# Kernel optimization log

Hardware: AMD Instinct MI355X
Metric: run time of the kernel (lower is better)

Reference implementation:

```python
import jax, jax.numpy as jnp
import numpy as np

B = 1048576
EPS = 1e-5

def _lin_params(key, din, dout):
    k1, k2 = jax.random.split(key)
    bound = 1.0 / np.sqrt(din)
    w = jax.random.uniform(k1, (din, dout), minval=-bound, maxval=bound, dtype=jnp.float32)
    b = jax.random.uniform(k2, (dout,), minval=-bound, maxval=bound, dtype=jnp.float32)
    return w, b

def setup_inputs() -> dict:
    key = jax.random.key(0)
    ks = jax.random.split(key, 10)
    x = jax.random.normal(ks[0], (B, 8), dtype=jnp.float32)
    dims = [(8, 16), (16, 16), (16, 12), (12, 8), (8, 4), (4, 4), (4, 4), (4, 1)]
    names = ['fm', 'c1', 'p1', 'c2', 'p2', 'c3', 'r', 'h']
    inp = {'x': x,
           'bn_g': jnp.ones((8,), jnp.float32),
           'bn_b': jnp.zeros((8,), jnp.float32)}
    for i, (nm, (di, do)) in enumerate(zip(names, dims)):
        w, b = _lin_params(ks[i + 1], di, do)
        inp['w_' + nm] = w
        inp['b_' + nm] = b
    return inp

def reference(x, bn_g, bn_b, w_fm, b_fm, w_c1, b_c1, w_p1, b_p1, w_c2, b_c2,
              w_p2, b_p2, w_c3, b_c3, w_r, b_r, w_h, b_h):
    # BatchNorm1d (training mode): batch statistics, biased variance
    mu = jnp.mean(x, axis=0)
    var = jnp.mean((x - mu) ** 2, axis=0)
    h = (x - mu) * jax.lax.rsqrt(var + EPS) * bn_g + bn_b
    h = jnp.tanh(h @ w_fm + b_fm)   # [B,16] feature_map
    h = jnp.tanh(h @ w_c1 + b_c1)   # [B,16] conv1
    h = jnp.tanh(h @ w_p1 + b_p1)   # [B,12] pool1
    h = jnp.tanh(h @ w_c2 + b_c2)   # [B,8]  conv2
    h = jnp.tanh(h @ w_p2 + b_p2)   # [B,4]  pool2
    h = jnp.tanh(h @ w_c3 + b_c3)   # [B,4]  conv3
    res = jax.nn.relu(h @ w_r + b_r)  # [B,4] residual branch
    h = h + res
    return jax.nn.sigmoid(h @ w_h + b_h)  # [B,1]
```

## Files before the change

### kernel.cpp

```cpp
#include <hip/hip_runtime.h>
#include <stdint.h>

#define B_ROWS 1048576
#define ROWS_PER_THREAD 2
#define MAIN_BLOCKS (B_ROWS / (256 * ROWS_PER_THREAD))
#define STAT_BLOCKS 1024

typedef __fp16 h2 __attribute__((ext_vector_type(2)));

#define PART_OFF 16
#define WPK_OFF 16400
#define BIA_OFF 16770
#define W_FM 0
#define W_C1 64
#define W_P1 192
#define W_C2 288
#define W_P2 336
#define W_C3 352
#define W_R  360
#define W_H  368
#define B_FM 0
#define B_C1 16
#define B_P1 32
#define B_C2 44
#define B_P2 52
#define B_C3 56
#define B_R  60
#define B_H  64

__device__ __forceinline__ float exp_tanh(float x) {
    float e = __builtin_amdgcn_exp2f(x * 2.8853900817779268f);
    return 1.0f - 2.0f * __builtin_amdgcn_rcpf(e + 1.0f);
}

__device__ __forceinline__ float fast_sigmoid(float x) {
    float e = __builtin_amdgcn_exp2f(x * -1.4426950408889634f);
    return __builtin_amdgcn_rcpf(1.0f + e);
}

__global__ __launch_bounds__(256) void bn_stats(const float* __restrict__ x,
                                                float* __restrict__ ws) {
    const int tid = blockIdx.x * 256 + threadIdx.x;
    float s[8], q[8];
#pragma unroll
    for (int c = 0; c < 8; ++c) { s[c] = 0.f; q[c] = 0.f; }
    const float4* x4 = (const float4*)x;
#pragma unroll
    for (int k = 0; k < 4; ++k) {
        int r = tid + k * 262144;
        float4 a = x4[2 * r];
        float4 b = x4[2 * r + 1];
        s[0] += a.x; s[1] += a.y; s[2] += a.z; s[3] += a.w;
        s[4] += b.x; s[5] += b.y; s[6] += b.z; s[7] += b.w;
        q[0] += a.x * a.x; q[1] += a.y * a.y; q[2] += a.z * a.z; q[3] += a.w * a.w;
        q[4] += b.x * b.x; q[5] += b.y * b.y; q[6] += b.z * b.z; q[7] += b.w * b.w;
    }
#pragma unroll
    for (int off = 32; off > 0; off >>= 1) {
#pragma unroll
        for (int c = 0; c < 8; ++c) {
            s[c] += __shfl_down(s[c], off);
            q[c] += __shfl_down(q[c], off);
        }
    }
    __shared__ float red[4][16];
    const int lane = threadIdx.x & 63;
    const int wave = threadIdx.x >> 6;
    if (lane == 0) {
#pragma unroll
        for (int c = 0; c < 8; ++c) { red[wave][c] = s[c]; red[wave][8 + c] = q[c]; }
    }
    __syncthreads();
    if (threadIdx.x < 16) {
        float acc = red[0][threadIdx.x] + red[1][threadIdx.x] +
                    red[2][threadIdx.x] + red[3][threadIdx.x];
        ws[PART_OFF + blockIdx.x * 16 + threadIdx.x] = acc;
    }
}

template<int DIN, int DOUT>
__device__ void pack_layer(const float* __restrict__ w, const float* __restrict__ b,
                           uint32_t* __restrict__ wdst, float* __restrict__ bdst,
                           const float* sc, const float* sh, bool fold) {
    for (int idx = threadIdx.x; idx < DOUT * (DIN / 2); idx += blockDim.x) {
        int j = idx / (DIN / 2), i2 = idx % (DIN / 2);
        float w0 = w[(2 * i2) * DOUT + j];
        float w1 = w[(2 * i2 + 1) * DOUT + j];
        if (fold) { w0 *= sc[2 * i2]; w1 *= sc[2 * i2 + 1]; }
        h2 h; h.x = (__fp16)w0; h.y = (__fp16)w1;
        wdst[j * (DIN / 2) + i2] = __builtin_bit_cast(uint32_t, h);
    }
    for (int j = threadIdx.x; j < DOUT; j += blockDim.x) {
        float bb = b[j];
        if (fold) {
#pragma unroll
            for (int i = 0; i < 8; ++i) bb += sh[i] * w[i * DOUT + j];
        }
        bdst[j] = bb;
    }
}

__global__ __launch_bounds__(256) void prep(
    float* __restrict__ ws,
    const float* __restrict__ bn_g, const float* __restrict__ bn_b,
    const float* __restrict__ w_fm, const float* __restrict__ b_fm,
    const float* __restrict__ w_c1, const float* __restrict__ b_c1,
    const float* __restrict__ w_p1, const float* __restrict__ b_p1,
    const float* __restrict__ w_c2, const float* __restrict__ b_c2,
    const float* __restrict__ w_p2, const float* __restrict__ b_p2,
    const float* __restrict__ w_c3, const float* __restrict__ b_c3,
    const float* __restrict__ w_r,  const float* __restrict__ b_r,
    const float* __restrict__ w_h,  const float* __restrict__ b_h)
{
    __shared__ float acc[16][17];
    __shared__ float scs[8], shs[8];
    {
        const int f = threadIdx.x & 15;
        const int chunk = threadIdx.x >> 4;
        float a = 0.f;
        const float* p = ws + PART_OFF + (chunk * 64) * 16 + f;
#pragma unroll 8
        for (int b = 0; b < 64; ++b) a += p[b * 16];
        acc[chunk][f] = a;
    }
    __syncthreads();
    if (threadIdx.x < 16) {
        float t = 0.f;
#pragma unroll
        for (int c = 0; c < 16; ++c) t += acc[c][threadIdx.x];
        acc[16 - 16][threadIdx.x] = t;
    }
    __syncthreads();
    if (threadIdx.x < 8) {
        const float invB = 1.0f / (float)B_ROWS;
        int c = threadIdx.x;
        float mu  = acc[0][c] * invB;
        float var = fmaf(-mu, mu, acc[0][8 + c] * invB);
        float s   = bn_g[c] * rsqrtf(var + 1e-5f);
        scs[c] = s;
        shs[c] = fmaf(-mu, s, bn_b[c]);
    }
    __syncthreads();
    uint32_t* wpk = (uint32_t*)(ws + WPK_OFF);
    float*    bpk = ws + BIA_OFF;
    pack_layer<8, 16>(w_fm, b_fm, wpk + W_FM, bpk + B_FM, scs, shs, true);
    pack_layer<16,16>(w_c1, b_c1, wpk + W_C1, bpk + B_C1, scs, shs, false);
    pack_layer<16,12>(w_p1, b_p1, wpk + W_P1, bpk + B_P1, scs, shs, false);
    pack_layer<12, 8>(w_c2, b_c2, wpk + W_C2, bpk + B_C2, scs, shs, false);
    pack_layer<8,  4>(w_p2, b_p2, wpk + W_P2, bpk + B_P2, scs, shs, false);
    pack_layer<4,  4>(w_c3, b_c3, wpk + W_C3, bpk + B_C3, scs, shs, false);
    pack_layer<4,  4>(w_r,  b_r,  wpk + W_R,  bpk + B_R,  scs, shs, false);
    pack_layer<4,  1>(w_h,  b_h,  wpk + W_H,  bpk + B_H,  scs, shs, false);
}

__device__ __forceinline__ float lut_tanh(float x, const float2* __restrict__ lut) {
    float t  = fmaf(x, 128.0f, 512.0f);
    t = __builtin_amdgcn_fmed3f(t, 0.0f, 1023.998f);
    float fl = floorf(t);
    float fr = t - fl;
    float2 e = lut[(int)fl];
    return fmaf(e.y, fr, e.x);
}

template<int DIN, int DOUT>
__device__ __forceinline__ void layer_dot(const h2* __restrict__ apkA, const h2* __restrict__ apkB,
                                          float* __restrict__ outA, float* __restrict__ outB,
                                          const uint32_t* __restrict__ wpk,
                                          const float* __restrict__ bias) {
#pragma unroll
    for (int j = 0; j < DOUT; ++j) {
        float accA = bias[j];
        float accB = accA;
#pragma unroll
        for (int i2 = 0; i2 < DIN / 2; ++i2) {
            h2 w = __builtin_bit_cast(h2, wpk[j * (DIN / 2) + i2]);
            accA = __builtin_amdgcn_fdot2(apkA[i2], w, accA, false);
            accB = __builtin_amdgcn_fdot2(apkB[i2], w, accB, false);
        }
        outA[j] = accA;
        outB[j] = accB;
    }
}

template<int N>
__device__ __forceinline__ void tanh_pack(const float* __restrict__ inA, const float* __restrict__ inB,
                                          h2* __restrict__ pkA, h2* __restrict__ pkB,
                                          const float2* __restrict__ lut) {
#pragma unroll
    for (int k = 0; k < N / 2; ++k) {
        float a0 = lut_tanh(inA[2 * k], lut);
        float a1 = lut_tanh(inA[2 * k + 1], lut);
        float b0 = lut_tanh(inB[2 * k], lut);
        float b1 = lut_tanh(inB[2 * k + 1], lut);
        pkA[k] = __builtin_amdgcn_cvt_pkrtz(a0, a1);
        pkB[k] = __builtin_amdgcn_cvt_pkrtz(b0, b1);
    }
}

__global__ __launch_bounds__(256) void qcnn_main(
    const float* __restrict__ x,
    const float* __restrict__ ws, float* __restrict__ out)
{
    const int tid = blockIdx.x * 256 + threadIdx.x;
    const int r0 = tid, r1 = tid + (B_ROWS / 2);
    const float4* x4 = (const float4*)x;
    float4 xa0 = x4[2 * r0], xa1 = x4[2 * r0 + 1];
    float4 xb0 = x4[2 * r1], xb1 = x4[2 * r1 + 1];

    __shared__ float2 lut[1024];
    {
        const float h = 0.0078125f;
#pragma unroll
        for (int k = 0; k < 4; ++k) {
            int i = threadIdx.x + k * 256;
            float x0 = fmaf((float)i, h, -4.0f);
            float t0 = exp_tanh(x0);
            float t1 = exp_tanh(x0 + h);
            lut[i] = make_float2(t0, t1 - t0);
        }
    }
    __syncthreads();

    const uint32_t* wpk = (const uint32_t*)(ws + WPK_OFF);
    const float*    bpk = ws + BIA_OFF;

    h2 a8[4], b8[4];
    a8[0] = __builtin_amdgcn_cvt_pkrtz(xa0.x, xa0.y);
    a8[1] = __builtin_amdgcn_cvt_pkrtz(xa0.z, xa0.w);
    a8[2] = __builtin_amdgcn_cvt_pkrtz(xa1.x, xa1.y);
    a8[3] = __builtin_amdgcn_cvt_pkrtz(xa1.z, xa1.w);
    b8[0] = __builtin_amdgcn_cvt_pkrtz(xb0.x, xb0.y);
    b8[1] = __builtin_amdgcn_cvt_pkrtz(xb0.z, xb0.w);
    b8[2] = __builtin_amdgcn_cvt_pkrtz(xb1.x, xb1.y);
    b8[3] = __builtin_amdgcn_cvt_pkrtz(xb1.z, xb1.w);

    float oA[16], oB[16]; h2 pA[8], pB[8];
    layer_dot<8, 16>(a8, b8, oA, oB, wpk + W_FM, bpk + B_FM);
    tanh_pack<16>(oA, oB, pA, pB, lut);
    float o2A[16], o2B[16]; h2 p2A[8], p2B[8];
    layer_dot<16,16>(pA, pB, o2A, o2B, wpk + W_C1, bpk + B_C1);
    tanh_pack<16>(o2A, o2B, p2A, p2B, lut);
    float o3A[12], o3B[12]; h2 p3A[6], p3B[6];
    layer_dot<16,12>(p2A, p2B, o3A, o3B, wpk + W_P1, bpk + B_P1);
    tanh_pack<12>(o3A, o3B, p3A, p3B, lut);
    float o4A[8], o4B[8]; h2 p4A[4], p4B[4];
    layer_dot<12, 8>(p3A, p3B, o4A, o4B, wpk + W_C2, bpk + B_C2);
    tanh_pack<8>(o4A, o4B, p4A, p4B, lut);
    float o5A[4], o5B[4]; h2 p5A[2], p5B[2];
    layer_dot<8,  4>(p4A, p4B, o5A, o5B, wpk + W_P2, bpk + B_P2);
    tanh_pack<4>(o5A, o5B, p5A, p5B, lut);
    float c4A[4], c4B[4];
    layer_dot<4,  4>(p5A, p5B, c4A, c4B, wpk + W_C3, bpk + B_C3);
#pragma unroll
    for (int j = 0; j < 4; ++j) {
        c4A[j] = lut_tanh(c4A[j], lut);
        c4B[j] = lut_tanh(c4B[j], lut);
    }
    h2 pcA[2], pcB[2];
    pcA[0] = __builtin_amdgcn_cvt_pkrtz(c4A[0], c4A[1]);
    pcA[1] = __builtin_amdgcn_cvt_pkrtz(c4A[2], c4A[3]);
    pcB[0] = __builtin_amdgcn_cvt_pkrtz(c4B[0], c4B[1]);
    pcB[1] = __builtin_amdgcn_cvt_pkrtz(c4B[2], c4B[3]);
    float r4A[4], r4B[4];
    layer_dot<4,  4>(pcA, pcB, r4A, r4B, wpk + W_R, bpk + B_R);
#pragma unroll
    for (int j = 0; j < 4; ++j) {
        c4A[j] += fmaxf(r4A[j], 0.f);
        c4B[j] += fmaxf(r4B[j], 0.f);
    }
    h2 phA[2], phB[2];
    phA[0] = __builtin_amdgcn_cvt_pkrtz(c4A[0], c4A[1]);
    phA[1] = __builtin_amdgcn_cvt_pkrtz(c4A[2], c4A[3]);
    phB[0] = __builtin_amdgcn_cvt_pkrtz(c4B[0], c4B[1]);
    phB[1] = __builtin_amdgcn_cvt_pkrtz(c4B[2], c4B[3]);
    float ohA[1], ohB[1];
    layer_dot<4,  1>(phA, phB, ohA, ohB, wpk + W_H, bpk + B_H);
    out[r0] = fast_sigmoid(ohA[0]);
    out[r1] = fast_sigmoid(ohB[0]);
}

extern "C" void kernel_launch(void* const* d_in, const int* in_sizes, int n_in,
                              void* d_out, int out_size, void* d_ws, size_t ws_size,
                              hipStream_t stream) {
    const float* x    = (const float*)d_in[0];
    const float* bn_g = (const float*)d_in[1];
    const float* bn_b = (const float*)d_in[2];
    const float* w_fm = (const float*)d_in[3];
    const float* b_fm = (const float*)d_in[4];
    const float* w_c1 = (const float*)d_in[5];
    const float* b_c1 = (const float*)d_in[6];
    const float* w_p1 = (const float*)d_in[7];
    const float* b_p1 = (const float*)d_in[8];
    const float* w_c2 = (const float*)d_in[9];
    const float* b_c2 = (const float*)d_in[10];
    const float* w_p2 = (const float*)d_in[11];
    const float* b_p2 = (const float*)d_in[12];
    const float* w_c3 = (const float*)d_in[13];
    const float* b_c3 = (const float*)d_in[14];
    const float* w_r  = (const float*)d_in[15];
    const float* b_r  = (const float*)d_in[16];
    const float* w_h  = (const float*)d_in[17];
    const float* b_h  = (const float*)d_in[18];
    float* out = (float*)d_out;
    float* ws  = (float*)d_ws;

    bn_stats<<<STAT_BLOCKS, 256, 0, stream>>>(x, ws);
    prep<<<1, 256, 0, stream>>>(ws, bn_g, bn_b, w_fm, b_fm, w_c1, b_c1, w_p1, b_p1,
                                w_c2, b_c2, w_p2, b_p2, w_c3, b_c3, w_r, b_r, w_h, b_h);
    qcnn_main<<<MAIN_BLOCKS, 256, 0, stream>>>(x, ws, out);
}
```

Baseline: 146.6 us.

## Eliminate prep kernel by folding weight packing into stats and BN finalize into main

Removes the single-block prep launch. Weight packing moves into block 0 of the stats kernel, and each main-kernel block now reduces the 512 partial sums itself to form BN scale and shift. Normalization is applied to the inputs in fp32 rather than folded into the first layer's weights. Stats blocks are halved with twice the rows per thread. This trades one serialized tiny launch for redundant per-block reduction work and two extra barriers in the main kernel.

```diff
diff --git a/kernel.cpp b/kernel.cpp
--- a/kernel.cpp
+++ b/kernel.cpp
@@ -2,15 +2,14 @@
 #include <stdint.h>
 
 #define B_ROWS 1048576
-#define ROWS_PER_THREAD 2
-#define MAIN_BLOCKS (B_ROWS / (256 * ROWS_PER_THREAD))
-#define STAT_BLOCKS 1024
+#define STAT_BLOCKS 512
+#define MAIN_BLOCKS 2048
 
 typedef __fp16 h2 __attribute__((ext_vector_type(2)));
 
 #define PART_OFF 16
-#define WPK_OFF 16400
-#define BIA_OFF 16770
+#define WPK_OFF 8208
+#define BIA_OFF 8578
 #define W_FM 0
 #define W_C1 64
 #define W_P1 192
@@ -38,71 +37,21 @@
     return __builtin_amdgcn_rcpf(1.0f + e);
 }
 
-__global__ __launch_bounds__(256) void bn_stats(const float* __restrict__ x,
-                                                float* __restrict__ ws) {
-    const int tid = blockIdx.x * 256 + threadIdx.x;
-    float s[8], q[8];
-#pragma unroll
-    for (int c = 0; c < 8; ++c) { s[c] = 0.f; q[c] = 0.f; }
-    const float4* x4 = (const float4*)x;
-#pragma unroll
-    for (int k = 0; k < 4; ++k) {
-        int r = tid + k * 262144;
-        float4 a = x4[2 * r];
-        float4 b = x4[2 * r + 1];
-        s[0] += a.x; s[1] += a.y; s[2] += a.z; s[3] += a.w;
-        s[4] += b.x; s[5] += b.y; s[6] += b.z; s[7] += b.w;
-        q[0] += a.x * a.x; q[1] += a.y * a.y; q[2] += a.z * a.z; q[3] += a.w * a.w;
-        q[4] += b.x * b.x; q[5] += b.y * b.y; q[6] += b.z * b.z; q[7] += b.w * b.w;
-    }
-#pragma unroll
-    for (int off = 32; off > 0; off >>= 1) {
-#pragma unroll
-        for (int c = 0; c < 8; ++c) {
-            s[c] += __shfl_down(s[c], off);
-            q[c] += __shfl_down(q[c], off);
-        }
-    }
-    __shared__ float red[4][16];
-    const int lane = threadIdx.x & 63;
-    const int wave = threadIdx.x >> 6;
-    if (lane == 0) {
-#pragma unroll
-        for (int c = 0; c < 8; ++c) { red[wave][c] = s[c]; red[wave][8 + c] = q[c]; }
-    }
-    __syncthreads();
-    if (threadIdx.x < 16) {
-        float acc = red[0][threadIdx.x] + red[1][threadIdx.x] +
-                    red[2][threadIdx.x] + red[3][threadIdx.x];
-        ws[PART_OFF + blockIdx.x * 16 + threadIdx.x] = acc;
-    }
-}
-
 template<int DIN, int DOUT>
 __device__ void pack_layer(const float* __restrict__ w, const float* __restrict__ b,
-                           uint32_t* __restrict__ wdst, float* __restrict__ bdst,
-                           const float* sc, const float* sh, bool fold) {
+                           uint32_t* __restrict__ wdst, float* __restrict__ bdst) {
     for (int idx = threadIdx.x; idx < DOUT * (DIN / 2); idx += blockDim.x) {
         int j = idx / (DIN / 2), i2 = idx % (DIN / 2);
-        float w0 = w[(2 * i2) * DOUT + j];
-        float w1 = w[(2 * i2 + 1) * DOUT + j];
-        if (fold) { w0 *= sc[2 * i2]; w1 *= sc[2 * i2 + 1]; }
-        h2 h; h.x = (__fp16)w0; h.y = (__fp16)w1;
+        h2 h;
+        h.x = (__fp16)w[(2 * i2) * DOUT + j];
+        h.y = (__fp16)w[(2 * i2 + 1) * DOUT + j];
         wdst[j * (DIN / 2) + i2] = __builtin_bit_cast(uint32_t, h);
     }
-    for (int j = threadIdx.x; j < DOUT; j += blockDim.x) {
-        float bb = b[j];
-        if (fold) {
-#pragma unroll
-            for (int i = 0; i < 8; ++i) bb += sh[i] * w[i * DOUT + j];
-        }
-        bdst[j] = bb;
-    }
-}
-
-__global__ __launch_bounds__(256) void prep(
-    float* __restrict__ ws,
-    const float* __restrict__ bn_g, const float* __restrict__ bn_b,
+    for (int j = threadIdx.x; j < DOUT; j += blockDim.x) bdst[j] = b[j];
+}
+
+__global__ __launch_bounds__(256) void bn_stats(
+    const float* __restrict__ x, float* __restrict__ ws,
     const float* __restrict__ w_fm, const float* __restrict__ b_fm,
     const float* __restrict__ w_c1, const float* __restrict__ b_c1,
     const float* __restrict__ w_p1, const float* __restrict__ b_p1,
@@ -112,45 +61,54 @@
     const float* __restrict__ w_r,  const float* __restrict__ b_r,
     const float* __restrict__ w_h,  const float* __restrict__ b_h)
 {
-    __shared__ float acc[16][17];
-    __shared__ float scs[8], shs[8];
-    {
-        const int f = threadIdx.x & 15;
-        const int chunk = threadIdx.x >> 4;
-        float a = 0.f;
-        const float* p = ws + PART_OFF + (chunk * 64) * 16 + f;
-#pragma unroll 8
-        for (int b = 0; b < 64; ++b) a += p[b * 16];
-        acc[chunk][f] = a;
+    const int tid = blockIdx.x * 256 + threadIdx.x;
+    float s[8], q[8];
+#pragma unroll
+    for (int c = 0; c < 8; ++c) { s[c] = 0.f; q[c] = 0.f; }
+    const float4* x4 = (const float4*)x;
+#pragma unroll
+    for (int k = 0; k < 8; ++k) {
+        int r = tid + k * 131072;
+        float4 a = x4[2 * r];
+        float4 b = x4[2 * r + 1];
+        s[0] += a.x; s[1] += a.y; s[2] += a.z; s[3] += a.w;
+        s[4] += b.x; s[5] += b.y; s[6] += b.z; s[7] += b.w;
+        q[0] += a.x * a.x; q[1] += a.y * a.y; q[2] += a.z * a.z; q[3] += a.w * a.w;
+        q[4] += b.x * b.x; q[5] += b.y * b.y; q[6] += b.z * b.z; q[7] += b.w * b.w;
+    }
+#pragma unroll
+    for (int off = 32; off > 0; off >>= 1) {
+#pragma unroll
+        for (int c = 0; c < 8; ++c) {
+            s[c] += __shfl_down(s[c], off);
+            q[c] += __shfl_down(q[c], off);
+        }
+    }
+    __shared__ float red[4][16];
+    const int lane = threadIdx.x & 63;
+    const int wave = threadIdx.x >> 6;
+    if (lane == 0) {
+#pragma unroll
+        for (int c = 0; c < 8; ++c) { red[wave][c] = s[c]; red[wave][8 + c] = q[c]; }
     }
     __syncthreads();
     if (threadIdx.x < 16) {
-        float t = 0.f;
-#pragma unroll
-        for (int c = 0; c < 16; ++c) t += acc[c][threadIdx.x];
-        acc[16 - 16][threadIdx.x] = t;
-    }
-    __syncthreads();
-    if (threadIdx.x < 8) {
-        const float invB = 1.0f / (float)B_ROWS;
-        int c = threadIdx.x;
-        float mu  = acc[0][c] * invB;
-        float var = fmaf(-mu, mu, acc[0][8 + c] * invB);
-        float s   = bn_g[c] * rsqrtf(var + 1e-5f);
-        scs[c] = s;
-        shs[c] = fmaf(-mu, s, bn_b[c]);
-    }
-    __syncthreads();
-    uint32_t* wpk = (uint32_t*)(ws + WPK_OFF);
-    float*    bpk = ws + BIA_OFF;
-    pack_layer<8, 16>(w_fm, b_fm, wpk + W_FM, bpk + B_FM, scs, shs, true);
-    pack_layer<16,16>(w_c1, b_c1, wpk + W_C1, bpk + B_C1, scs, shs, false);
-    pack_layer<16,12>(w_p1, b_p1, wpk + W_P1, bpk + B_P1, scs, shs, false);
-    pack_layer<12, 8>(w_c2, b_c2, wpk + W_C2, bpk + B_C2, scs, shs, false);
-    pack_layer<8,  4>(w_p2, b_p2, wpk + W_P2, bpk + B_P2, scs, shs, false);
-    pack_layer<4,  4>(w_c3, b_c3, wpk + W_C3, bpk + B_C3, scs, shs, false);
-    pack_layer<4,  4>(w_r,  b_r,  wpk + W_R,  bpk + B_R,  scs, shs, false);
-    pack_layer<4,  1>(w_h,  b_h,  wpk + W_H,  bpk + B_H,  scs, shs, false);
+        float acc = red[0][threadIdx.x] + red[1][threadIdx.x] +
+                    red[2][threadIdx.x] + red[3][threadIdx.x];
+        ws[PART_OFF + blockIdx.x * 16 + threadIdx.x] = acc;
+    }
+    if (blockIdx.x == 0) {
+        uint32_t* wpk = (uint32_t*)(ws + WPK_OFF);
+        float*    bpk = ws + BIA_OFF;
+        pack_layer<8, 16>(w_fm, b_fm, wpk + W_FM, bpk + B_FM);
+        pack_layer<16,16>(w_c1, b_c1, wpk + W_C1, bpk + B_C1);
+        pack_layer<16,12>(w_p1, b_p1, wpk + W_P1, bpk + B_P1);
+        pack_layer<12, 8>(w_c2, b_c2, wpk + W_C2, bpk + B_C2);
+        pack_layer<8,  4>(w_p2, b_p2, wpk + W_P2, bpk + B_P2);
+        pack_layer<4,  4>(w_c3, b_c3, wpk + W_C3, bpk + B_C3);
+        pack_layer<4,  4>(w_r,  b_r,  wpk + W_R,  bpk + B_R);
+        pack_layer<4,  1>(w_h,  b_h,  wpk + W_H,  bpk + B_H);
+    }
 }
 
 __device__ __forceinline__ float lut_tanh(float x, const float2* __restrict__ lut) {
@@ -199,6 +157,7 @@
 
 __global__ __launch_bounds__(256) void qcnn_main(
     const float* __restrict__ x,
+    const float* __restrict__ bn_g, const float* __restrict__ bn_b,
     const float* __restrict__ ws, float* __restrict__ out)
 {
     const int tid = blockIdx.x * 256 + threadIdx.x;
@@ -208,6 +167,9 @@
     float4 xb0 = x4[2 * r1], xb1 = x4[2 * r1 + 1];
 
     __shared__ float2 lut[1024];
+    __shared__ float accs[16][17];
+    __shared__ float scs[8], shs[8];
+
     {
         const float h = 0.0078125f;
 #pragma unroll
@@ -219,20 +181,56 @@
             lut[i] = make_float2(t0, t1 - t0);
         }
     }
+    {
+        const int f = threadIdx.x & 15;
+        const int chunk = threadIdx.x >> 4;
+        const float* p = ws + PART_OFF + (chunk * 32) * 16 + f;
+        float a = 0.f;
+#pragma unroll 8
+        for (int b = 0; b < 32; ++b) a += p[b * 16];
+        accs[chunk][f] = a;
+    }
     __syncthreads();
+    if (threadIdx.x < 16) {
+        float t = 0.f;
+#pragma unroll
+        for (int c = 0; c < 16; ++c) t += accs[c][threadIdx.x];
+        accs[0][threadIdx.x] = t;
+    }
+    __syncthreads();
+    if (threadIdx.x < 8) {
+        const float invB = 1.0f / (float)B_ROWS;
+        int c = threadIdx.x;
+        float mu  = accs[0][c] * invB;
+        float var = fmaf(-mu, mu, accs[0][8 + c] * invB);
+        float s   = bn_g[c] * rsqrtf(var + 1e-5f);
+        scs[c] = s;
+        shs[c] = fmaf(-mu, s, bn_b[c]);
+    }
+    __syncthreads();
+
+    float sc[8], sh[8];
+#pragma unroll
+    for (int c = 0; c < 8; ++c) { sc[c] = scs[c]; sh[c] = shs[c]; }
 
     const uint32_t* wpk = (const uint32_t*)(ws + WPK_OFF);
     const float*    bpk = ws + BIA_OFF;
 
+    float nA[8], nB[8];
+    nA[0] = fmaf(xa0.x, sc[0], sh[0]); nA[1] = fmaf(xa0.y, sc[1], sh[1]);
+    nA[2] = fmaf(xa0.z, sc[2], sh[2]); nA[3] = fmaf(xa0.w, sc[3], sh[3]);
+    nA[4] = fmaf(xa1.x, sc[4], sh[4]); nA[5] = fmaf(xa1.y, sc[5], sh[5]);
+    nA[6] = fmaf(xa1.z, sc[6], sh[6]); nA[7] = fmaf(xa1.w, sc[7], sh[7]);
+    nB[0] = fmaf(xb0.x, sc[0], sh[0]); nB[1] = fmaf(xb0.y, sc[1], sh[1]);
+    nB[2] = fmaf(xb0.z, sc[2], sh[2]); nB[3] = fmaf(xb0.w, sc[3], sh[3]);
+    nB[4] = fmaf(xb1.x, sc[4], sh[4]); nB[5] = fmaf(xb1.y, sc[5], sh[5]);
+    nB[6] = fmaf(xb1.z, sc[6], sh[6]); nB[7] = fmaf(xb1.w, sc[7], sh[7]);
     h2 a8[4], b8[4];
-    a8[0] = __builtin_amdgcn_cvt_pkrtz(xa0.x, xa0.y);
-    a8[1] = __builtin_amdgcn_cvt_pkrtz(xa0.z, xa0.w);
-    a8[2] = __builtin_amdgcn_cvt_pkrtz(xa1.x, xa1.y);
-    a8[3] = __builtin_amdgcn_cvt_pkrtz(xa1.z, xa1.w);
-    b8[0] = __builtin_amdgcn_cvt_pkrtz(xb0.x, xb0.y);
-    b8[1] = __builtin_amdgcn_cvt_pkrtz(xb0.z, xb0.w);
-    b8[2] = __builtin_amdgcn_cvt_pkrtz(xb1.x, xb1.y);
-    b8[3] = __builtin_amdgcn_cvt_pkrtz(xb1.z, xb1.w);
+#pragma unroll
+    for (int k = 0; k < 4; ++k) {
+        a8[k] = __builtin_amdgcn_cvt_pkrtz(nA[2 * k], nA[2 * k + 1]);
+        b8[k] = __builtin_amdgcn_cvt_pkrtz(nB[2 * k], nB[2 * k + 1]);
+    }
 
     float oA[16], oB[16]; h2 pA[8], pB[8];
     layer_dot<8, 16>(a8, b8, oA, oB, wpk + W_FM, bpk + B_FM);
@@ -304,8 +302,8 @@
     float* out = (float*)d_out;
     float* ws  = (float*)d_ws;
 
-    bn_stats<<<STAT_BLOCKS, 256, 0, stream>>>(x, ws);
-    prep<<<1, 256, 0, stream>>>(ws, bn_g, bn_b, w_fm, b_fm, w_c1, b_c1, w_p1, b_p1,
-                                w_c2, b_c2, w_p2, b_p2, w_c3, b_c3, w_r, b_r, w_h, b_h);
-    qcnn_main<<<MAIN_BLOCKS, 256, 0, stream>>>(x, ws, out);
-}
+    bn_stats<<<STAT_BLOCKS, 256, 0, stream>>>(
+        x, ws, w_fm, b_fm, w_c1, b_c1, w_p1, b_p1, w_c2, b_c2,
+        w_p2, b_p2, w_c3, b_c3, w_r, b_r, w_h, b_h);
+    qcnn_main<<<MAIN_BLOCKS, 256, 0, stream>>>(x, bn_g, bn_b, ws, out);
+}
```

Measured after the change: 143.1 us. -2.4%, faster.
